# Performance work log

Measured on AMD Instinct MI355X. Metric: run time of the kernel, lower is better.

Reference implementation:

```python
import jax, jax.numpy as jnp
import numpy as np

# Config constants (mirror EnergyConfig)
MIN_CARD = 26.0
CARD_PEN = 25.0
PLANE_W = 1.0
FACET_W = 8.0
RANK_EPS = 1e-6
BOUND_W = 4.0
SUP_W = 1.0
ACT_W = 1.0
INACT_W = 0.35
MARGIN = 0.05
PROB_POW = 1.0
PLANE_TOPK = 128
ACTIVE_TOPK = 64

N_POINTS, DIM, BATCH = 65536, 8, 256


def _topk_filter(w, k):
    # Keep only the top-k entries per row, zero elsewhere (scatter of gathered values).
    if k <= 0 or k >= w.shape[-1]:
        return w
    vals, idx = jax.lax.top_k(w, k)
    rows = jnp.arange(w.shape[0])[:, None]
    return jnp.zeros_like(w).at[rows, idx].set(vals)


def setup_inputs() -> dict:
    key = jax.random.key(0)
    k1, k2 = jax.random.split(key)
    probabilities = jax.random.uniform(k1, (BATCH, N_POINTS), dtype=jnp.float32)
    points = jax.random.normal(k2, (N_POINTS, DIM), dtype=jnp.float32)
    return {"probabilities": probabilities, "points": points}


def reference(probabilities, points):
    prob = jnp.clip(probabilities, 1e-5, 1.0 - 1e-5)  # (B,N)

    # ---- weighted plane statistics (weighted PCA) ----
    pw = _topk_filter(prob, PLANE_TOPK)                       # (B,N)
    wsum = jnp.clip(pw.sum(-1), 1e-6)                          # (B,)
    mean = (pw @ points) / wsum[:, None]                       # (B,D)
    pp = points[:, :, None] * points[:, None, :]               # (N,D,D), small since D=8
    second_moment = jnp.einsum('bn,nij->bij', pw, pp) / wsum[:, None, None]
    cov = second_moment - mean[:, :, None] * mean[:, None, :]  # (B,D,D)
    cov = 0.5 * (cov + cov.swapaxes(1, 2))
    eigvals, eigvecs = jnp.linalg.eigh(cov)                    # ascending
    plane_term = eigvals[:, 0]
    second_eig = eigvals[:, 1]
    facet_term = plane_term / (second_eig + RANK_EPS)
    normal = eigvecs[:, :, 0]                                  # (B,D) smallest-eig direction

    # ---- dual-orientation boundary terms ----
    proj = points @ normal.T                                   # (N,B)
    active_w = _topk_filter(prob ** PROB_POW, ACTIVE_TOPK)     # (B,N)
    active_norm = jnp.clip(active_w.sum(-1), 1e-6)
    inactive_w = 1.0 - prob
    inactive_norm = jnp.clip(inactive_w.sum(-1), 1e-6)

    def orientation_boundary(p):
        # p: (N,B) oriented projections
        offset = -p.max(axis=0)                                # (B,)
        signed = p + offset[None, :]                           # (N,B), max is 0
        sb = signed.T                                          # (B,N)
        active_res = sb * sb                                   # quadratic active loss
        active = (active_w * active_res).sum(-1) / active_norm
        slack = jax.nn.relu(MARGIN + sb)
        inactive = (inactive_w * slack * slack).sum(-1) / inactive_norm
        support = jax.nn.relu(signed.max(axis=0)) ** 2
        return SUP_W * support + ACT_W * active + INACT_W * inactive

    b_pos = orientation_boundary(proj)
    b_neg = orientation_boundary(-proj)
    boundary = jnp.where(b_pos <= b_neg, b_pos, b_neg)

    # ---- cardinality penalty ----
    cardinality = prob.sum(-1)
    deficit = jax.nn.relu(MIN_CARD - cardinality)
    card_term = CARD_PEN * deficit * deficit

    total = PLANE_W * plane_term + FACET_W * facet_term + BOUND_W * boundary + card_term
    return total
```

## Files before the change

### kernel.cpp

```cpp
#include <hip/hip_runtime.h>
#include <cstdint>
#include <cstddef>

constexpr int NPTS   = 65536;
constexpr int B      = 256;
constexpr int CHUNKS = 8;
constexpr int CHUNK  = NPTS / CHUNKS;
constexpr int CCAP   = 160;
constexpr int NBLK   = B * CHUNKS;
constexpr int NEARCAP = 256;

constexpr size_t WSO_CBUF    = 0;
constexpr size_t WSO_NEAR    = WSO_CBUF + (size_t)NBLK * CCAP * 2;
constexpr size_t WSO_NEARCNT = WSO_NEAR + (size_t)2 * B * NEARCAP * 2;
constexpr size_t WSO_PSUM    = WSO_NEARCNT + 2 * B;
constexpr size_t WSO_CCNT    = WSO_PSUM + NBLK;
constexpr size_t WSO_PLANE   = WSO_CCNT + NBLK;
constexpr size_t WSO_FACET   = WSO_PLANE + B;
constexpr size_t WSO_NRM     = WSO_FACET + B;
constexpr size_t WSO_SUMP    = WSO_NRM + (size_t)B * 8;
constexpr size_t WSO_ANORM   = WSO_SUMP + B;
constexpr size_t WSO_T64V    = WSO_ANORM + B;
constexpr size_t WSO_T64I    = WSO_T64V + (size_t)B * 64;
constexpr size_t WSO_PMAXP   = WSO_T64I + (size_t)B * 64;
constexpr size_t WSO_PMAXN   = WSO_PMAXP + B;

__device__ __forceinline__ float clipp(float x) {
    return fminf(fmaxf(x, 1e-5f), 0.99999f);
}
__device__ __forceinline__ unsigned f2mono(float f) {
    unsigned u = __float_as_uint(f);
    return (u & 0x80000000u) ? ~u : (u | 0x80000000u);
}
__device__ __forceinline__ float mono2f(unsigned e) {
    return __uint_as_float((e & 0x80000000u) ? (e ^ 0x80000000u) : ~e);
}
__device__ __forceinline__ int cand_bin(float v) {
    int b = (int)((v - 0.99f) * 102400.0f);
    return min(max(b, 0), 1023);
}
__device__ __forceinline__ float dot8(float4 a, float4 b, const float* n) {
    float d = a.x * n[0];
    d = fmaf(a.y, n[1], d); d = fmaf(a.z, n[2], d); d = fmaf(a.w, n[3], d);
    d = fmaf(b.x, n[4], d); d = fmaf(b.y, n[5], d); d = fmaf(b.z, n[6], d);
    d = fmaf(b.w, n[7], d);
    return d;
}

__global__ __launch_bounds__(256) void kA_stream(
    const float* __restrict__ prob, float* __restrict__ ws)
{
    __shared__ float wred[4];
    __shared__ int lcnt;
    const int tid   = threadIdx.x;
    const int row   = blockIdx.x >> 3;
    const int chunk = blockIdx.x & 7;
    if (tid == 0) lcnt = 0;
    __syncthreads();

    unsigned long long* cb = (unsigned long long*)ws + (size_t)blockIdx.x * CCAP;
    const float4* p4 = (const float4*)(prob + (size_t)row * NPTS + (size_t)chunk * CHUNK);

    float4 v[8];
    #pragma unroll
    for (int i = 0; i < 8; i++) v[i] = p4[i * 256 + tid];

    float lsum = 0.f;
    #pragma unroll
    for (int i = 0; i < 8; i++) {
        float c0 = clipp(v[i].x), c1 = clipp(v[i].y), c2 = clipp(v[i].z), c3 = clipp(v[i].w);
        lsum += (c0 + c1) + (c2 + c3);
        float mx = fmaxf(fmaxf(c0, c1), fmaxf(c2, c3));
        if (mx >= 0.99f) {
            int bi = chunk * CHUNK + (i * 256 + tid) * 4;
            float c4[4] = {c0, c1, c2, c3};
            #pragma unroll
            for (int j = 0; j < 4; j++) {
                if (c4[j] >= 0.99f) {
                    int p_ = atomicAdd(&lcnt, 1);
                    if (p_ < CCAP)
                        cb[p_] = (((unsigned long long)__float_as_uint(c4[j])) << 32)
                               | (unsigned)~(bi + j);
                }
            }
        }
    }
    #pragma unroll
    for (int off = 32; off; off >>= 1) lsum += __shfl_down(lsum, off);
    if ((tid & 63) == 0) wred[tid >> 6] = lsum;
    __syncthreads();
    if (tid == 0) {
        ws[WSO_PSUM + blockIdx.x] = (wred[0] + wred[1]) + (wred[2] + wred[3]);
        ((int*)ws)[WSO_CCNT + blockIdx.x] = min(lcnt, CCAP);
    }
}

constexpr int CSLOTS = CHUNKS * CCAP;
constexpr int GITER  = CSLOTS / 256;
__global__ __launch_bounds__(256) void kB_select(
    const float* __restrict__ points, float* __restrict__ ws)
{
    __shared__ unsigned long long cand[CSLOTS];
    __shared__ unsigned long long comp[256];
    __shared__ int   hist[1024];
    __shared__ int   counts_s[CHUNKS];
    __shared__ int   ccnt_s, bt_s;
    __shared__ float sw[128];
    __shared__ float pc[128][9];
    __shared__ float sred[44][4];
    __shared__ float slotm[44];
    __shared__ float wpart[2];
    __shared__ float covm[64];

    const int row = blockIdx.x;
    const int tid = threadIdx.x;

    if (tid < CHUNKS) counts_s[tid] = ((const int*)ws)[WSO_CCNT + row * CHUNKS + tid];
    if (tid == 0) { ccnt_s = 0; bt_s = 0; }
    #pragma unroll
    for (int k = 0; k < 4; k++) hist[tid * 4 + k] = 0;
    __syncthreads();

    const unsigned long long* cb = (const unsigned long long*)ws;
    #pragma unroll
    for (int r = 0; r < GITER; r++) {
        int s = r * 256 + tid;
        int c = s / CCAP, t = s - c * CCAP;
        unsigned long long k = 0ull;
        if (t < counts_s[c]) {
            k = cb[(size_t)(row * CHUNKS + c) * CCAP + t];
            atomicAdd(&hist[cand_bin(__uint_as_float((unsigned)(k >> 32)))], 1);
        }
        cand[s] = k;
    }
    __syncthreads();

    if (tid < 64) {
        int h[16]; int g = 0;
        #pragma unroll
        for (int k = 0; k < 16; k++) { h[k] = hist[tid * 16 + k]; g += h[k]; }
        int s = g;
        #pragma unroll
        for (int off = 1; off < 64; off <<= 1) {
            int o = __shfl_down(s, off);
            if (tid + off < 64) s += o;
        }
        int Snext = __shfl_down(s, 1);
        if (tid == 63) Snext = 0;
        if (s >= 128 && Snext < 128) {
            int acc = Snext, bt = tid * 16;
            #pragma unroll
            for (int k = 15; k >= 0; k--) {
                acc += h[k];
                if (acc >= 128) { bt = tid * 16 + k; break; }
            }
            bt_s = bt;
        }
    }
    __syncthreads();

    const int bt = bt_s;
    #pragma unroll
    for (int r = 0; r < GITER; r++) {
        unsigned long long k = cand[r * 256 + tid];
        if (k && cand_bin(__uint_as_float((unsigned)(k >> 32))) >= bt) {
            int p_ = atomicAdd(&ccnt_s, 1);
            if (p_ < 256) comp[p_] = k;
        }
    }
    __syncthreads();
    const int m = min(ccnt_s, 256);

    if (tid < 128) {
        sw[tid] = 0.f;
        #pragma unroll
        for (int j = 0; j < 9; j++) pc[tid][j] = (j == 8) ? 1.f : 0.f;
    }
    if (tid < 64) {
        ws[WSO_T64V + (size_t)row * 64 + tid] = 0.f;
        ((int*)ws)[WSO_T64I + (size_t)row * 64 + tid] = 0;
    }
    unsigned long long ki = (tid < m) ? comp[tid] : 0ull;
    int rank = 0;
    for (int j = 0; j < m; j++) rank += (comp[j] > ki) ? 1 : 0;
    __syncthreads();

    if (tid < m && rank < 128) {
        float v = __uint_as_float((unsigned)(ki >> 32));
        unsigned idx = ~(unsigned)(ki & 0xFFFFFFFFu);
        sw[rank] = v;
        const float4* pt = (const float4*)(points + (size_t)idx * 8);
        float4 q0 = pt[0], q1 = pt[1];
        pc[rank][0] = q0.x; pc[rank][1] = q0.y; pc[rank][2] = q0.z; pc[rank][3] = q0.w;
        pc[rank][4] = q1.x; pc[rank][5] = q1.y; pc[rank][6] = q1.z; pc[rank][7] = q1.w;
        if (rank < 64) {
            ws[WSO_T64V + (size_t)row * 64 + rank] = v;
            ((int*)ws)[WSO_T64I + (size_t)row * 64 + rank] = (int)idx;
        }
    }
    __syncthreads();

    if (tid < 128) {
        float ww = sw[tid];
        #pragma unroll
        for (int off = 32; off; off >>= 1) ww += __shfl_down(ww, off);
        if ((tid & 63) == 0) wpart[tid >> 6] = ww;
    }
    if (tid < 176) {
        int s = tid >> 2, part = tid & 3;
        int i_, j_;
        if (s < 36) {
            int rem = s; i_ = 0;
            while (rem >= 8 - i_) { rem -= 8 - i_; i_++; }
            j_ = i_ + rem;
        } else { i_ = s - 36; j_ = 8; }
        float acc = 0.f;
        for (int k = part * 32; k < part * 32 + 32; k++)
            acc += sw[k] * pc[k][i_] * pc[k][j_];
        sred[s][part] = acc;
    }
    __syncthreads();
    if (tid < 44) slotm[tid] = (sred[tid][0] + sred[tid][1]) + (sred[tid][2] + sred[tid][3]);
    __syncthreads();

    if (tid < 64) {
        float w128 = fmaxf(wpart[0] + wpart[1], 1e-6f);
        int i_ = tid >> 3, j_ = tid & 7;
        int a_ = min(i_, j_), b_ = max(i_, j_);
        int s3 = 8 * a_ - (a_ * (a_ - 1)) / 2 + (b_ - a_);
        covm[tid] = slotm[s3] / w128 - (slotm[36 + i_] / w128) * (slotm[36 + j_] / w128);
    }
    __syncthreads();

    if (tid == 64) {
        ws[WSO_ANORM + row] = fmaxf(wpart[0], 1e-6f);
        float s = 0.f;
        for (int c = 0; c < CHUNKS; c++) s += ws[WSO_PSUM + row * CHUNKS + c];
        ws[WSO_SUMP + row] = s;
        ((unsigned*)ws)[WSO_PMAXP + row] = 0u;
        ((unsigned*)ws)[WSO_PMAXN + row] = 0u;
        ((int*)ws)[WSO_NEARCNT + row * 2 + 0] = 0;
        ((int*)ws)[WSO_NEARCNT + row * 2 + 1] = 0;
    }

    if (tid < 64) {
        const int i = tid >> 3, j = tid & 7;
        float a = covm[tid];
        float v = (i == j) ? 1.f : 0.f;
        const unsigned PR[7] = {023456701u, 001234567u, 050712346u, 034067125u,
                                012305674u, 067120453u, 045671032u};
        #pragma unroll 1
        for (int sweep = 0; sweep < 6; sweep++) {
            #pragma unroll
            for (int r = 0; r < 7; r++) {
                const unsigned pk = PR[r];
                const int rp = (pk >> (3 * i)) & 7;
                const int cp = (pk >> (3 * j)) & 7;
                const int pr = min(i, rp), qr = max(i, rp);
                float app = __shfl(a, pr * 9);
                float aqq = __shfl(a, qr * 9);
                float apq = __shfl(a, pr * 8 + qr);
                float tau = 0.5f * (aqq - app);
                float den = fabsf(tau) + sqrtf(fmaf(tau, tau, apq * apq));
                float t = __fdividef(apq, den + 1e-38f);
                t = (tau < 0.f) ? -t : t;
                float cr = rsqrtf(fmaf(t, t, 1.f));
                float sr = t * cr;
                float cc = __shfl(cr, j * 9);
                float sc = __shfl(sr, j * 9);
                float oth = __shfl(a, rp * 8 + j);
                a = fmaf((i < rp) ? -sr : sr, oth, cr * a);
                float oth2 = __shfl(a, i * 8 + cp);
                a = fmaf((j < cp) ? -sc : sc, oth2, cc * a);
                float ov = __shfl(v, i * 8 + cp);
                v = fmaf((j < cp) ? -sc : sc, ov, cc * v);
            }
        }
        float d[8];
        #pragma unroll
        for (int k = 0; k < 8; k++) d[k] = __shfl(a, k * 9);
        float e0 = d[0]; int i0 = 0;
        #pragma unroll
        for (int k = 1; k < 8; k++) if (d[k] < e0) { e0 = d[k]; i0 = k; }
        float e1 = 3.4e38f;
        #pragma unroll
        for (int k = 0; k < 8; k++) if (k != i0 && d[k] < e1) e1 = d[k];
        if (tid == 0) {
            ws[WSO_PLANE + row] = e0;
            ws[WSO_FACET + row] = e0 / (e1 + 1e-6f);
        }
        if (j == i0) ws[WSO_NRM + (size_t)row * 8 + i] = v;
    }
}

constexpr int R3 = 4;
constexpr int P3 = 2048;
__global__ __launch_bounds__(256) void k3a_max(
    const float* __restrict__ points, float* __restrict__ ws)
{
    __shared__ float redp[4][R3], redn[4][R3];
    __shared__ float bmax[2 * R3];
    const int tid = threadIdx.x;
    const int r0  = blockIdx.y * R3;
    const int n0  = blockIdx.x * P3;
    float nr[R3][8];
    #pragma unroll
    for (int r = 0; r < R3; r++)
        #pragma unroll
        for (int j = 0; j < 8; j++)
            nr[r][j] = ws[WSO_NRM + (size_t)(r0 + r) * 8 + j];
    float dsv[P3 / 256][R3];
    float mp[R3], mn[R3];
    #pragma unroll
    for (int r = 0; r < R3; r++) { mp[r] = -3.4e38f; mn[r] = -3.4e38f; }
    const float4* pb = (const float4*)points + (size_t)n0 * 2;
    #pragma unroll
    for (int it = 0; it < P3 / 256; it++) {
        int t2 = (it * 256 + tid) * 2;
        float4 q0 = pb[t2], q1 = pb[t2 + 1];
        #pragma unroll
        for (int r = 0; r < R3; r++) {
            float d = dot8(q0, q1, nr[r]);
            dsv[it][r] = d;
            mp[r] = fmaxf(mp[r], d);
            mn[r] = fmaxf(mn[r], -d);
        }
    }
    #pragma unroll
    for (int r = 0; r < R3; r++) {
        #pragma unroll
        for (int off = 32; off; off >>= 1) {
            mp[r] = fmaxf(mp[r], __shfl_xor(mp[r], off));
            mn[r] = fmaxf(mn[r], __shfl_xor(mn[r], off));
        }
    }
    if ((tid & 63) == 0) {
        int wv = tid >> 6;
        #pragma unroll
        for (int r = 0; r < R3; r++) { redp[wv][r] = mp[r]; redn[wv][r] = mn[r]; }
    }
    __syncthreads();
    if (tid < 2 * R3) {
        int r = tid & (R3 - 1);
        bool neg = tid >= R3;
        float m = neg
            ? fmaxf(fmaxf(redn[0][r], redn[1][r]), fmaxf(redn[2][r], redn[3][r]))
            : fmaxf(fmaxf(redp[0][r], redp[1][r]), fmaxf(redp[2][r], redp[3][r]));
        bmax[tid] = m;
        unsigned* wsu = (unsigned*)ws;
        atomicMax(&wsu[(neg ? WSO_PMAXN : WSO_PMAXP) + r0 + r], f2mono(m));
    }
    __syncthreads();
    float bmx[R3], bmn[R3];
    #pragma unroll
    for (int r = 0; r < R3; r++) { bmx[r] = bmax[r]; bmn[r] = bmax[R3 + r]; }

    int* ncnt = (int*)ws + WSO_NEARCNT;
    unsigned long long* nbuf = (unsigned long long*)ws + WSO_NEAR / 2;
    #pragma unroll
    for (int it = 0; it < P3 / 256; it++) {
        int nn = n0 + it * 256 + tid;
        #pragma unroll
        for (int r = 0; r < R3; r++) {
            float d = dsv[it][r];
            if (d >= bmx[r] - 0.05f) {
                int p_ = atomicAdd(&ncnt[(r0 + r) * 2 + 0], 1);
                if (p_ < NEARCAP)
                    nbuf[(size_t)((r0 + r) * 2 + 0) * NEARCAP + p_] =
                        (((unsigned long long)__float_as_uint(d)) << 32) | (unsigned)nn;
            }
            if (-d >= bmn[r] - 0.05f) {
                int p_ = atomicAdd(&ncnt[(r0 + r) * 2 + 1], 1);
                if (p_ < NEARCAP)
                    nbuf[(size_t)((r0 + r) * 2 + 1) * NEARCAP + p_] =
                        (((unsigned long long)__float_as_uint(-d)) << 32) | (unsigned)nn;
            }
        }
    }
}

__global__ __launch_bounds__(64) void k3cd_final(
    const float* __restrict__ points, const float* __restrict__ prob,
    const float* __restrict__ ws, float* __restrict__ out)
{
    const int row = blockIdx.x;
    const int t   = threadIdx.x;
    const unsigned* wsu = (const unsigned*)ws;
    __shared__ float nl[8];
    if (t < 8) nl[t] = ws[WSO_NRM + (size_t)row * 8 + t];
    __syncthreads();

    const float pmaxp = mono2f(wsu[WSO_PMAXP + row]);
    const float pmaxn = mono2f(wsu[WSO_PMAXN + row]);

    float w   = ws[WSO_T64V + (size_t)row * 64 + t];
    int   idx = ((const int*)ws)[WSO_T64I + (size_t)row * 64 + t];
    const float4* pt = (const float4*)(points + (size_t)idx * 8);
    float4 q0 = pt[0], q1 = pt[1];
    float d = dot8(q0, q1, nl);
    float sp = d - pmaxp, sn = -d - pmaxn;
    float ap = w * sp * sp;
    float an = w * sn * sn;

    const int* ncnt = (const int*)ws + WSO_NEARCNT;
    const unsigned long long* nbuf = (const unsigned long long*)ws + WSO_NEAR / 2;
    float ip = 0.f, in_ = 0.f;
    int cp = min(ncnt[row * 2 + 0], NEARCAP);
    int cn = min(ncnt[row * 2 + 1], NEARCAP);
    for (int i = t; i < cp; i += 64) {
        unsigned long long e = nbuf[(size_t)(row * 2 + 0) * NEARCAP + i];
        float dv = __uint_as_float((unsigned)(e >> 32));
        float tp = 0.05f + (dv - pmaxp);
        if (tp > 0.f) {
            float w2 = 1.0f - clipp(prob[(size_t)row * NPTS + (unsigned)(e & 0xFFFFFFFFu)]);
            ip = fmaf(w2 * tp, tp, ip);
        }
    }
    for (int i = t; i < cn; i += 64) {
        unsigned long long e = nbuf[(size_t)(row * 2 + 1) * NEARCAP + i];
        float dv = __uint_as_float((unsigned)(e >> 32));
        float tn = 0.05f + (dv - pmaxn);
        if (tn > 0.f) {
            float w2 = 1.0f - clipp(prob[(size_t)row * NPTS + (unsigned)(e & 0xFFFFFFFFu)]);
            in_ = fmaf(w2 * tn, tn, in_);
        }
    }
    #pragma unroll
    for (int off = 32; off; off >>= 1) {
        ap  += __shfl_down(ap, off);
        an  += __shfl_down(an, off);
        ip  += __shfl_down(ip, off);
        in_ += __shfl_down(in_, off);
    }
    if (t == 0) {
        float anorm = ws[WSO_ANORM + row];
        float sump  = ws[WSO_SUMP + row];
        float inorm = fmaxf((float)NPTS - sump, 1e-6f);
        float bp = (ap / anorm) + 0.35f * (ip / inorm);
        float bn = (an / anorm) + 0.35f * (in_ / inorm);
        float bd = (bp <= bn) ? bp : bn;
        float def = fmaxf(26.0f - sump, 0.f);
        out[row] = ws[WSO_PLANE + row] + 8.0f * ws[WSO_FACET + row]
                 + 4.0f * bd + 25.0f * def * def;
    }
}

extern "C" void kernel_launch(void* const* d_in, const int* in_sizes, int n_in,
                              void* d_out, int out_size, void* d_ws, size_t ws_size,
                              hipStream_t stream) {
    const float* prob   = (const float*)d_in[0];
    const float* points = (const float*)d_in[1];
    float* out = (float*)d_out;
    float* ws  = (float*)d_ws;

    kA_stream<<<NBLK, 256, 0, stream>>>(prob, ws);
    kB_select<<<B, 256, 0, stream>>>(points, ws);
    dim3 g3(NPTS / P3, B / R3);
    k3a_max<<<g3, 256, 0, stream>>>(points, ws);
    k3cd_final<<<B, 64, 0, stream>>>(points, prob, ws, out);
}
```

Baseline: 144.4 us.

## Split projection max and near-candidate collection into two passes with global threshold

The fused max-and-candidate kernel is split into two kernels. The first computes projections of a 256-point tile against 128 normals staged in LDS and reduces per-row maxima with global atomicMax. The second recomputes the projections and collects near-maximum candidates against the global threshold instead of a block-local one, which is meant to cut candidate atomics and overflow of the near buffer. In exchange, points are read and dot products computed twice, there is an extra launch, and many more blocks issue atomicMax on the same per-row addresses.

```diff
diff --git a/kernel.cpp b/kernel.cpp
--- a/kernel.cpp
+++ b/kernel.cpp
@@ -293,87 +293,108 @@
     }
 }
 
-constexpr int R3 = 4;
-constexpr int P3 = 2048;
+constexpr int PBLK = 256;
 __global__ __launch_bounds__(256) void k3a_max(
     const float* __restrict__ points, float* __restrict__ ws)
 {
-    __shared__ float redp[4][R3], redn[4][R3];
-    __shared__ float bmax[2 * R3];
-    const int tid = threadIdx.x;
-    const int r0  = blockIdx.y * R3;
-    const int n0  = blockIdx.x * P3;
-    float nr[R3][8];
-    #pragma unroll
-    for (int r = 0; r < R3; r++)
-        #pragma unroll
-        for (int j = 0; j < 8; j++)
-            nr[r][j] = ws[WSO_NRM + (size_t)(r0 + r) * 8 + j];
-    float dsv[P3 / 256][R3];
-    float mp[R3], mn[R3];
-    #pragma unroll
-    for (int r = 0; r < R3; r++) { mp[r] = -3.4e38f; mn[r] = -3.4e38f; }
-    const float4* pb = (const float4*)points + (size_t)n0 * 2;
-    #pragma unroll
-    for (int it = 0; it < P3 / 256; it++) {
-        int t2 = (it * 256 + tid) * 2;
-        float4 q0 = pb[t2], q1 = pb[t2 + 1];
-        #pragma unroll
-        for (int r = 0; r < R3; r++) {
-            float d = dot8(q0, q1, nr[r]);
-            dsv[it][r] = d;
-            mp[r] = fmaxf(mp[r], d);
-            mn[r] = fmaxf(mn[r], -d);
-        }
-    }
-    #pragma unroll
-    for (int r = 0; r < R3; r++) {
+    __shared__ float nlds[128][8];
+    const int tid  = threadIdx.x;
+    const int lane = tid & 63;
+    const int wv   = tid >> 6;
+    const int pb   = blockIdx.x;
+    const int rh   = blockIdx.y;
+
+    ((float4*)nlds)[tid] = ((const float4*)(ws + WSO_NRM))[rh * 256 + tid];
+
+    float4 q[4][2];
+    const float4* pp = (const float4*)points + (size_t)pb * (PBLK * 2);
+    #pragma unroll
+    for (int j = 0; j < 4; j++) {
+        q[j][0] = pp[(j * 64 + lane) * 2];
+        q[j][1] = pp[(j * 64 + lane) * 2 + 1];
+    }
+    __syncthreads();
+
+    unsigned* wsu = (unsigned*)ws;
+    #pragma unroll 2
+    for (int rr = 0; rr < 32; rr++) {
+        int r  = (rr + pb) & 31;
+        int lr = wv * 32 + r;
+        float4 n0 = *(const float4*)&nlds[lr][0];
+        float4 n1 = *(const float4*)&nlds[lr][4];
+        float nn[8] = {n0.x, n0.y, n0.z, n0.w, n1.x, n1.y, n1.z, n1.w};
+        float mp = -3.4e38f, mn = -3.4e38f;
+        #pragma unroll
+        for (int j = 0; j < 4; j++) {
+            float d = dot8(q[j][0], q[j][1], nn);
+            mp = fmaxf(mp, d);
+            mn = fmaxf(mn, -d);
+        }
         #pragma unroll
         for (int off = 32; off; off >>= 1) {
-            mp[r] = fmaxf(mp[r], __shfl_xor(mp[r], off));
-            mn[r] = fmaxf(mn[r], __shfl_xor(mn[r], off));
-        }
-    }
-    if ((tid & 63) == 0) {
-        int wv = tid >> 6;
-        #pragma unroll
-        for (int r = 0; r < R3; r++) { redp[wv][r] = mp[r]; redn[wv][r] = mn[r]; }
-    }
-    __syncthreads();
-    if (tid < 2 * R3) {
-        int r = tid & (R3 - 1);
-        bool neg = tid >= R3;
-        float m = neg
-            ? fmaxf(fmaxf(redn[0][r], redn[1][r]), fmaxf(redn[2][r], redn[3][r]))
-            : fmaxf(fmaxf(redp[0][r], redp[1][r]), fmaxf(redp[2][r], redp[3][r]));
-        bmax[tid] = m;
-        unsigned* wsu = (unsigned*)ws;
-        atomicMax(&wsu[(neg ? WSO_PMAXN : WSO_PMAXP) + r0 + r], f2mono(m));
-    }
-    __syncthreads();
-    float bmx[R3], bmn[R3];
-    #pragma unroll
-    for (int r = 0; r < R3; r++) { bmx[r] = bmax[r]; bmn[r] = bmax[R3 + r]; }
+            mp = fmaxf(mp, __shfl_xor(mp, off));
+            mn = fmaxf(mn, __shfl_xor(mn, off));
+        }
+        if (lane == 0) {
+            int gr = rh * 128 + lr;
+            atomicMax(&wsu[WSO_PMAXP + gr], f2mono(mp));
+            atomicMax(&wsu[WSO_PMAXN + gr], f2mono(mn));
+        }
+    }
+}
+
+__global__ __launch_bounds__(256) void k3b_near(
+    const float* __restrict__ points, float* __restrict__ ws)
+{
+    __shared__ float nlds[128][8];
+    __shared__ float thp[128], thn[128];
+    const int tid  = threadIdx.x;
+    const int lane = tid & 63;
+    const int wv   = tid >> 6;
+    const int pb   = blockIdx.x;
+    const int rh   = blockIdx.y;
+    const unsigned* wsu = (const unsigned*)ws;
+
+    ((float4*)nlds)[tid] = ((const float4*)(ws + WSO_NRM))[rh * 256 + tid];
+    if (tid < 128) {
+        thp[tid] = mono2f(wsu[WSO_PMAXP + rh * 128 + tid]) - 0.05f;
+        thn[tid] = mono2f(wsu[WSO_PMAXN + rh * 128 + tid]) - 0.05f;
+    }
+
+    float4 q[4][2];
+    const float4* pp = (const float4*)points + (size_t)pb * (PBLK * 2);
+    #pragma unroll
+    for (int j = 0; j < 4; j++) {
+        q[j][0] = pp[(j * 64 + lane) * 2];
+        q[j][1] = pp[(j * 64 + lane) * 2 + 1];
+    }
+    __syncthreads();
 
     int* ncnt = (int*)ws + WSO_NEARCNT;
     unsigned long long* nbuf = (unsigned long long*)ws + WSO_NEAR / 2;
-    #pragma unroll
-    for (int it = 0; it < P3 / 256; it++) {
-        int nn = n0 + it * 256 + tid;
-        #pragma unroll
-        for (int r = 0; r < R3; r++) {
-            float d = dsv[it][r];
-            if (d >= bmx[r] - 0.05f) {
-                int p_ = atomicAdd(&ncnt[(r0 + r) * 2 + 0], 1);
+    #pragma unroll 2
+    for (int rr = 0; rr < 32; rr++) {
+        int lr = wv * 32 + rr;
+        int gr = rh * 128 + lr;
+        float4 n0 = *(const float4*)&nlds[lr][0];
+        float4 n1 = *(const float4*)&nlds[lr][4];
+        float nn[8] = {n0.x, n0.y, n0.z, n0.w, n1.x, n1.y, n1.z, n1.w};
+        float tp = thp[lr], tn = thn[lr];
+        #pragma unroll
+        for (int j = 0; j < 4; j++) {
+            float d = dot8(q[j][0], q[j][1], nn);
+            int nidx = pb * PBLK + j * 64 + lane;
+            if (d >= tp) {
+                int p_ = atomicAdd(&ncnt[gr * 2 + 0], 1);
                 if (p_ < NEARCAP)
-                    nbuf[(size_t)((r0 + r) * 2 + 0) * NEARCAP + p_] =
-                        (((unsigned long long)__float_as_uint(d)) << 32) | (unsigned)nn;
+                    nbuf[(size_t)(gr * 2 + 0) * NEARCAP + p_] =
+                        (((unsigned long long)__float_as_uint(d)) << 32) | (unsigned)nidx;
             }
-            if (-d >= bmn[r] - 0.05f) {
-                int p_ = atomicAdd(&ncnt[(r0 + r) * 2 + 1], 1);
+            if (-d >= tn) {
+                int p_ = atomicAdd(&ncnt[gr * 2 + 1], 1);
                 if (p_ < NEARCAP)
-                    nbuf[(size_t)((r0 + r) * 2 + 1) * NEARCAP + p_] =
-                        (((unsigned long long)__float_as_uint(-d)) << 32) | (unsigned)nn;
+                    nbuf[(size_t)(gr * 2 + 1) * NEARCAP + p_] =
+                        (((unsigned long long)__float_as_uint(-d)) << 32) | (unsigned)nidx;
             }
         }
     }
@@ -455,7 +476,8 @@
 
     kA_stream<<<NBLK, 256, 0, stream>>>(prob, ws);
     kB_select<<<B, 256, 0, stream>>>(points, ws);
-    dim3 g3(NPTS / P3, B / R3);
-    k3a_max<<<g3, 256, 0, stream>>>(points, ws);
+    dim3 gm(NPTS / PBLK, 2);
+    k3a_max<<<gm, 256, 0, stream>>>(points, ws);
+    k3b_near<<<gm, 256, 0, stream>>>(points, ws);
     k3cd_final<<<B, 64, 0, stream>>>(points, prob, ws, out);
 }
```

Result: slower. 209.7 us (+45.2%).
